# Performance work log

Measured on AMD Instinct MI355X. Metric: run time of the kernel, lower is better.

## Reference

```python
import jax, jax.numpy as jnp
import numpy as np

B, M, L, LQ, E, V = 32, 100, 30, 30, 256, 32000


def position_encoding(seq_len, emb):
    # faithful to MemN2N position encoding: 1 + 4*(k - (E+1)/2)*(j - (J+1)/2)/(E*J)
    j = jnp.arange(1, seq_len + 1, dtype=jnp.float32)[:, None]   # (J,1)
    k = jnp.arange(1, emb + 1, dtype=jnp.float32)[None, :]       # (1,E)
    half_e = (emb + 1) / 2.0
    half_j = (seq_len + 1) / 2.0
    return 1.0 + 4.0 * (k - half_e) * (j - half_j) / (emb * seq_len)  # (J,E)


def masked_softmax(x, m):
    xm = jnp.where(m > 0, x, -1e30)
    e = jnp.exp(xm - jnp.max(xm, axis=-1, keepdims=True)) * m
    return e / (jnp.sum(e, axis=-1, keepdims=True) + 1e-13)


def masked_log_softmax(x, m):
    return jax.nn.log_softmax(x + jnp.log(m + 1e-13), axis=-1)


def _forward(trainS, trainQ, trainVM, trainPM, trainSM, trainQM,
             A1, A2, A3, A4, W, b, gamma, beta):
    # query encoding: embed + position encode + query mask + sum over words
    Q = trainQ[:, 0, :]                                   # (B,LQ)
    pe_q = position_encoding(LQ, E)                       # (LQ,E)
    u = jnp.sum(A1[Q] * pe_q * trainQM[:, :, None], axis=1)  # (B,E)

    # story memory embeddings: gather + PE + sum over words.
    # NOTE: original code multiplies by trainSM but discards the result (bug),
    # so SM is intentionally NOT applied here.
    pe_s = position_encoding(L, E)                        # (L,E)
    embA1 = jnp.sum(A1[trainS] * pe_s, axis=2)            # (B,M,E)
    embA2 = jnp.sum(A2[trainS] * pe_s, axis=2)
    embA3 = jnp.sum(A3[trainS] * pe_s, axis=2)
    embA4 = jnp.sum(A4[trainS] * pe_s, axis=2)

    def hop(memA, memC, u):
        # scores = sum_E(memA * u) * PM (PM applied pre-sum is equivalent)
        scores = jnp.einsum('bme,be->bm', memA, u) * trainPM
        p = masked_softmax(scores, trainPM)               # (B,M)
        o = jnp.einsum('bm,bme->be', p, memC)             # (B,E)
        return o + u

    u = hop(embA1, embA2, u)   # hop 1
    u = hop(embA2, embA3, u)   # hop 2
    u = hop(embA3, embA4, u)   # hop 3

    # final linear + BatchNorm1d (training-mode batch stats, eps=1e-5)
    wx = u @ W.T + b                                      # (B,V)
    mean = jnp.mean(wx, axis=0)
    var = jnp.mean((wx - mean) ** 2, axis=0)
    y = gamma * (wx - mean) / jnp.sqrt(var + 1e-5) + beta
    return masked_log_softmax(y, trainVM)


def setup_inputs() -> dict:
    key = jax.random.key(0)
    ks = jax.random.split(key, 8)
    inp = {
        'trainS': jax.random.randint(ks[0], (B, M, L), 0, V, dtype=jnp.int32),
        'trainQ': jax.random.randint(ks[1], (B, 1, LQ), 0, V, dtype=jnp.int32),
        'trainVM': jnp.ones((B, V), jnp.float32),
        'trainPM': jnp.ones((B, M), jnp.float32),
        'trainSM': jnp.ones((B, M, L), jnp.float32),
        'trainQM': jnp.ones((B, LQ), jnp.float32),
        'A1': 0.1 * jax.random.normal(ks[2], (V, E), jnp.float32),
        'A2': 0.1 * jax.random.normal(ks[3], (V, E), jnp.float32),
        'A3': 0.1 * jax.random.normal(ks[4], (V, E), jnp.float32),
        'A4': 0.1 * jax.random.normal(ks[5], (V, E), jnp.float32),
        'W': jax.random.normal(ks[6], (V, E), jnp.float32) / np.sqrt(E),
        'b': jnp.zeros((V,), jnp.float32),
        'gamma': jnp.ones((V,), jnp.float32),
        'beta': jnp.zeros((V,), jnp.float32),
        'inspect': 0,
    }
    return inp


def reference(trainS, trainQ, trainVM, trainPM, trainSM, trainQM,
              A1, A2, A3, A4, W, b, gamma, beta, inspect):
    return _forward(trainS, trainQ, trainVM, trainPM, trainSM, trainQM,
                    A1, A2, A3, A4, W, b, gamma, beta)
```

## Files before the change

### kernel.cpp

```cpp
#include <hip/hip_runtime.h>
#include <math.h>

static constexpr int B_ = 32, M_ = 100, L_ = 30, LQ_ = 30, E_ = 256, V_ = 32000;

typedef __attribute__((ext_vector_type(8))) short bf16x8;
typedef __attribute__((ext_vector_type(4))) float f32x4;

__device__ __forceinline__ unsigned f2bf(float f) {
    unsigned u = __float_as_uint(f);
    return (u + 0x7FFFu + ((u >> 16) & 1u)) >> 16;
}

__global__ __launch_bounds__(256) void k_embed(const int* __restrict__ trainS,
                                               const float* __restrict__ A1,
                                               const float* __restrict__ A2,
                                               const float* __restrict__ A3,
                                               const float* __restrict__ A4,
                                               float* __restrict__ embA) {
    const int bm = blockIdx.x;
    const int tbl = threadIdx.x >> 6;
    const int e0 = (threadIdx.x & 63) * 4;
    const float* __restrict__ A = (tbl == 0) ? A1 : (tbl == 1) ? A2 : (tbl == 2) ? A3 : A4;
    const float half_e = (E_ + 1) * 0.5f;
    const float half_j = (L_ + 1) * 0.5f;
    const float inv = 1.0f / (float)(E_ * L_);
    const float k0 = (float)(e0 + 1) - half_e;
    const float k1 = k0 + 1.f, k2 = k0 + 2.f, k3 = k0 + 3.f;

    int idx[L_];
#pragma unroll
    for (int l = 0; l < L_; ++l) idx[l] = trainS[bm * L_ + l];

    float4 acc = make_float4(0.f, 0.f, 0.f, 0.f);
#pragma unroll
    for (int c = 0; c < 2; ++c) {
        float4 r[15];
#pragma unroll
        for (int j = 0; j < 15; ++j)
            r[j] = *reinterpret_cast<const float4*>(A + (size_t)idx[c * 15 + j] * E_ + e0);
        __builtin_amdgcn_sched_barrier(0);
#pragma unroll
        for (int j = 0; j < 15; ++j) {
            const int l = c * 15 + j;
            const float coef = 4.0f * ((float)(l + 1) - half_j) * inv;
            acc.x += r[j].x * (1.0f + coef * k0);
            acc.y += r[j].y * (1.0f + coef * k1);
            acc.z += r[j].z * (1.0f + coef * k2);
            acc.w += r[j].w * (1.0f + coef * k3);
        }
    }
    *reinterpret_cast<float4*>(embA + (size_t)tbl * (B_ * M_ * E_) + (size_t)bm * E_ + e0) = acc;
}

__global__ __launch_bounds__(1024) void k_hops(const int* __restrict__ trainQ,
                                               const float* __restrict__ trainQM,
                                               const float* __restrict__ A1,
                                               const float* __restrict__ embA,
                                               const float* __restrict__ trainPM,
                                               float* __restrict__ u_N,
                                               float* __restrict__ partial) {
    const int b = blockIdx.x;
    const int tid = threadIdx.x;
    const int lane = tid & 63;
    const int wave = tid >> 6;
    const int g = tid >> 8;
    const int e = tid & 255;
    if (tid < 8) partial[b * 8 + tid] = 0.f;
    __shared__ float u_sh[E_];
    __shared__ float sc[M_];
    __shared__ float p_sh[M_];
    __shared__ float osum[4][E_];

    {
        const float half_e = (E_ + 1) * 0.5f;
        const float half_j = (LQ_ + 1) * 0.5f;
        const float inv = 1.0f / (float)(E_ * LQ_);
        const float ke = (float)(e + 1) - half_e;
        const int l0 = g * 8;
        const int ln = (LQ_ - l0 < 8) ? (LQ_ - l0) : 8;
        int qi[8];
        float qm[8];
#pragma unroll
        for (int j = 0; j < 8; ++j) {
            if (j < ln) {
                qi[j] = trainQ[b * LQ_ + l0 + j];
                qm[j] = trainQM[b * LQ_ + l0 + j];
            } else { qi[j] = 0; qm[j] = 0.f; }
        }
        float r[8];
#pragma unroll
        for (int j = 0; j < 8; ++j)
            r[j] = (j < ln) ? A1[(size_t)qi[j] * E_ + e] : 0.f;
        float part = 0.f;
#pragma unroll
        for (int j = 0; j < 8; ++j) {
            const float pe = 1.0f + 4.0f * ke * ((float)(l0 + j + 1) - half_j) * inv;
            part += r[j] * pe * qm[j];
        }
        osum[g][e] = part;
    }
    __syncthreads();
    if (tid < E_) u_sh[tid] = osum[0][tid] + osum[1][tid] + osum[2][tid] + osum[3][tid];
    __syncthreads();

    for (int hop = 0; hop < 3; ++hop) {
        const float* memA = embA + (size_t)hop * (B_ * M_ * E_) + (size_t)b * M_ * E_;
        const float* memC = memA + (size_t)(B_ * M_ * E_);
#pragma unroll 2
        for (int m = wave; m < M_; m += 16) {
            const float* row = memA + m * E_;
            float part = 0.f;
#pragma unroll
            for (int j = 0; j < 4; ++j)
                part += row[lane + 64 * j] * u_sh[lane + 64 * j];
#pragma unroll
            for (int off = 32; off > 0; off >>= 1)
                part += __shfl_xor(part, off, 64);
            if (lane == 0) sc[m] = part * trainPM[b * M_ + m];
        }
        __syncthreads();
        if (wave == 0) {
            const float pm0 = (lane < M_) ? trainPM[b * M_ + lane] : 0.f;
            const float pm1 = (lane + 64 < M_) ? trainPM[b * M_ + lane + 64] : 0.f;
            const float x0 = (lane < M_ && pm0 > 0.f) ? sc[lane] : -1e30f;
            const float x1 = (lane + 64 < M_ && pm1 > 0.f) ? sc[lane + 64] : -1e30f;
            float mx = fmaxf(x0, x1);
#pragma unroll
            for (int off = 32; off > 0; off >>= 1)
                mx = fmaxf(mx, __shfl_xor(mx, off, 64));
            const float e0v = (lane < M_) ? expf(x0 - mx) * pm0 : 0.f;
            const float e1v = (lane + 64 < M_) ? expf(x1 - mx) * pm1 : 0.f;
            float ssum = e0v + e1v;
#pragma unroll
            for (int off = 32; off > 0; off >>= 1)
                ssum += __shfl_xor(ssum, off, 64);
            const float invs = 1.0f / (ssum + 1e-13f);
            if (lane < M_) p_sh[lane] = e0v * invs;
            if (lane + 64 < M_) p_sh[lane + 64] = e1v * invs;
        }
        __syncthreads();
        {
            float acc = 0.f;
            const float* crow = memC + e;
            const int m0 = g * 25;
#pragma unroll 5
            for (int mm = 0; mm < 25; ++mm)
                acc += p_sh[m0 + mm] * crow[(size_t)(m0 + mm) * E_];
            osum[g][e] = acc;
        }
        __syncthreads();
        if (tid < E_) u_sh[tid] += osum[0][tid] + osum[1][tid] + osum[2][tid] + osum[3][tid];
        __syncthreads();
    }
    if (tid < E_) u_N[b * E_ + tid] = u_sh[tid];
}

__global__ __launch_bounds__(256) void k_output(const float* __restrict__ u_N,
                                                const float* __restrict__ Wm,
                                                const float* __restrict__ gamma,
                                                const float* __restrict__ beta,
                                                const float* __restrict__ VM,
                                                float* __restrict__ z,
                                                float* __restrict__ partial) {
    __shared__ char uAraw[32 * 512];
    __shared__ float pex[B_];
    const int tid = threadIdx.x;
    {
        const int m = tid >> 3;
        const int kc = (tid & 7) * 32;
        const float4* src = reinterpret_cast<const float4*>(u_N + m * E_ + kc);
#pragma unroll
        for (int j = 0; j < 4; ++j) {
            const float4 f0 = src[2 * j];
            const float4 f1 = src[2 * j + 1];
            uint4 q;
            q.x = f2bf(f0.x) | (f2bf(f0.y) << 16);
            q.y = f2bf(f0.z) | (f2bf(f0.w) << 16);
            q.z = f2bf(f1.x) | (f2bf(f1.y) << 16);
            q.w = f2bf(f1.z) | (f2bf(f1.w) << 16);
            const int k16 = kc / 8 + j;
            const int off = m * 512 + ((k16 * 16) ^ ((m & 7) << 4));
            *reinterpret_cast<uint4*>(uAraw + off) = q;
        }
    }
    if (tid < B_) pex[tid] = 0.f;
    __syncthreads();

    const int lane = tid & 63;
    const int wv = tid >> 6;
    const int col = lane & 15;
    const int grp = lane >> 4;
    const int n0 = (blockIdx.x * 4 + wv) * 16;
    const int v = n0 + col;

    float4 wreg[16];
    {
        const float* wrow = Wm + (size_t)v * E_ + grp * 8;
#pragma unroll
        for (int s = 0; s < 8; ++s) {
            wreg[2 * s] = *reinterpret_cast<const float4*>(wrow + s * 32);
            wreg[2 * s + 1] = *reinterpret_cast<const float4*>(wrow + s * 32 + 4);
        }
    }
    __builtin_amdgcn_sched_barrier(0);

    bf16x8 af[2][8];
#pragma unroll
    for (int mt = 0; mt < 2; ++mt) {
        const int m = mt * 16 + col;
#pragma unroll
        for (int s = 0; s < 8; ++s) {
            const int k16 = s * 4 + grp;
            const int off = m * 512 + ((k16 * 16) ^ ((m & 7) << 4));
            af[mt][s] = *reinterpret_cast<bf16x8*>(uAraw + off);
        }
    }

    f32x4 acc0 = {0.f, 0.f, 0.f, 0.f};
    f32x4 acc1 = {0.f, 0.f, 0.f, 0.f};
#pragma unroll
    for (int s = 0; s < 8; ++s) {
        const float4 w0 = wreg[2 * s], w1 = wreg[2 * s + 1];
        bf16x8 bf;
        bf[0] = (short)f2bf(w0.x); bf[1] = (short)f2bf(w0.y);
        bf[2] = (short)f2bf(w0.z); bf[3] = (short)f2bf(w0.w);
        bf[4] = (short)f2bf(w1.x); bf[5] = (short)f2bf(w1.y);
        bf[6] = (short)f2bf(w1.z); bf[7] = (short)f2bf(w1.w);
        acc0 = __builtin_amdgcn_mfma_f32_16x16x32_bf16(af[0][s], bf, acc0, 0, 0, 0);
        acc1 = __builtin_amdgcn_mfma_f32_16x16x32_bf16(af[1][s], bf, acc1, 0, 0, 0);
    }

    float s1 = 0.f, s2 = 0.f;
#pragma unroll
    for (int r = 0; r < 4; ++r) {
        s1 += acc0[r] + acc1[r];
        s2 += acc0[r] * acc0[r] + acc1[r] * acc1[r];
    }
    s1 += __shfl_xor(s1, 16, 64);
    s2 += __shfl_xor(s2, 16, 64);
    s1 += __shfl_xor(s1, 32, 64);
    s2 += __shfl_xor(s2, 32, 64);
    const float mean = s1 * (1.0f / B_);
    const float var = s2 * (1.0f / B_) - mean * mean;
    const float rstd = rsqrtf(var + 1e-5f);
    const float gg = gamma[v], be = beta[v];

#pragma unroll
    for (int mt = 0; mt < 2; ++mt) {
#pragma unroll
        for (int r = 0; r < 4; ++r) {
            const int b = mt * 16 + grp * 4 + r;
            const float wx = (mt == 0) ? acc0[r] : acc1[r];
            const float y = gg * (wx - mean) * rstd + be;
            const size_t row = (size_t)b * V_ + v;
            const float vm = VM[row] + 1e-13f;
            z[row] = y + logf(vm);
            atomicAdd(&pex[b], vm * expf(y));
        }
    }
    __syncthreads();
    if (tid < B_) atomicAdd(&partial[tid * 8 + (blockIdx.x & 7)], pex[tid]);
}

__global__ __launch_bounds__(256) void k_final(const float* __restrict__ z,
                                               const float* __restrict__ partial,
                                               float* __restrict__ out) {
    const int idx = blockIdx.x * 256 + threadIdx.x;
    const int b = idx / (V_ / 4);
    const int v4 = idx % (V_ / 4);
    float s = 0.f;
#pragma unroll
    for (int k = 0; k < 8; ++k) s += partial[b * 8 + k];
    const float lse = logf(s);
    const float4 x = reinterpret_cast<const float4*>(z + (size_t)b * V_)[v4];
    float4 o;
    o.x = x.x - lse; o.y = x.y - lse; o.z = x.z - lse; o.w = x.w - lse;
    reinterpret_cast<float4*>(out + (size_t)b * V_)[v4] = o;
}

extern "C" void kernel_launch(void* const* d_in, const int* in_sizes, int n_in,
                              void* d_out, int out_size, void* d_ws, size_t ws_size,
                              hipStream_t stream) {
    const int* trainS = (const int*)d_in[0];
    const int* trainQ = (const int*)d_in[1];
    const float* trainVM = (const float*)d_in[2];
    const float* trainPM = (const float*)d_in[3];
    const float* trainQM = (const float*)d_in[5];
    const float* A1 = (const float*)d_in[6];
    const float* A2 = (const float*)d_in[7];
    const float* A3 = (const float*)d_in[8];
    const float* A4 = (const float*)d_in[9];
    const float* Wm = (const float*)d_in[10];
    const float* gamma = (const float*)d_in[12];
    const float* beta = (const float*)d_in[13];
    float* out = (float*)d_out;

    float* ws = (float*)d_ws;
    float* u_N = ws;
    float* embA = ws + 8192;
    float* z = embA + 4 * (B_ * M_ * E_);
    float* partial = z + (size_t)B_ * V_;

    k_embed<<<B_ * M_, 256, 0, stream>>>(trainS, A1, A2, A3, A4, embA);
    k_hops<<<B_, 1024, 0, stream>>>(trainQ, trainQM, A1, embA, trainPM, u_N, partial);
    k_output<<<V_ / 64, 256, 0, stream>>>(u_N, Wm, gamma, beta, trainVM, z, partial);
    k_final<<<(B_ * V_ / 4) / 256, 256, 0, stream>>>(z, partial, out);
}
```

Before: 108.9 us.

## Split output GEMM batch halves across waves and reduce exp sums via shuffles

In k_output, each block now covers 32 vocab columns instead of 64, and each wave computes one 16-row batch half of one 16-column tile. This doubles the grid and halves the per-wave MFMA and epilogue work. BatchNorm statistics are combined across wave pairs through shared memory with an extra barrier. The per-element shared-memory atomics for the softmax denominator are replaced by shuffle reductions followed by one atomic per row group. The trade-off is that each W row is now loaded by two waves, adding redundant global traffic, plus the added block-level sync.

New measurement: 118.2 us. 1.09x slower.

```diff
diff --git a/kernel.cpp b/kernel.cpp
--- a/kernel.cpp
+++ b/kernel.cpp
@@ -164,6 +164,7 @@
                                                 float* __restrict__ partial) {
     __shared__ char uAraw[32 * 512];
     __shared__ float pex[B_];
+    __shared__ float pairStat[2][2][16][2];
     const int tid = threadIdx.x;
     {
         const int m = tid >> 3;
@@ -188,10 +189,11 @@
 
     const int lane = tid & 63;
     const int wv = tid >> 6;
+    const int p = wv >> 1;
+    const int mt = wv & 1;
     const int col = lane & 15;
     const int grp = lane >> 4;
-    const int n0 = (blockIdx.x * 4 + wv) * 16;
-    const int v = n0 + col;
+    const int v = blockIdx.x * 32 + p * 16 + col;
 
     float4 wreg[16];
     {
@@ -204,20 +206,18 @@
     }
     __builtin_amdgcn_sched_barrier(0);
 
-    bf16x8 af[2][8];
-#pragma unroll
-    for (int mt = 0; mt < 2; ++mt) {
+    bf16x8 af[8];
+    {
         const int m = mt * 16 + col;
 #pragma unroll
         for (int s = 0; s < 8; ++s) {
             const int k16 = s * 4 + grp;
             const int off = m * 512 + ((k16 * 16) ^ ((m & 7) << 4));
-            af[mt][s] = *reinterpret_cast<bf16x8*>(uAraw + off);
-        }
-    }
-
-    f32x4 acc0 = {0.f, 0.f, 0.f, 0.f};
-    f32x4 acc1 = {0.f, 0.f, 0.f, 0.f};
+            af[s] = *reinterpret_cast<bf16x8*>(uAraw + off);
+        }
+    }
+
+    f32x4 acc = {0.f, 0.f, 0.f, 0.f};
 #pragma unroll
     for (int s = 0; s < 8; ++s) {
         const float4 w0 = wreg[2 * s], w1 = wreg[2 * s + 1];
@@ -226,37 +226,46 @@
         bf[2] = (short)f2bf(w0.z); bf[3] = (short)f2bf(w0.w);
         bf[4] = (short)f2bf(w1.x); bf[5] = (short)f2bf(w1.y);
         bf[6] = (short)f2bf(w1.z); bf[7] = (short)f2bf(w1.w);
-        acc0 = __builtin_amdgcn_mfma_f32_16x16x32_bf16(af[0][s], bf, acc0, 0, 0, 0);
-        acc1 = __builtin_amdgcn_mfma_f32_16x16x32_bf16(af[1][s], bf, acc1, 0, 0, 0);
-    }
-
-    float s1 = 0.f, s2 = 0.f;
-#pragma unroll
-    for (int r = 0; r < 4; ++r) {
-        s1 += acc0[r] + acc1[r];
-        s2 += acc0[r] * acc0[r] + acc1[r] * acc1[r];
-    }
+        acc = __builtin_amdgcn_mfma_f32_16x16x32_bf16(af[s], bf, acc, 0, 0, 0);
+    }
+
+    float s1 = acc[0] + acc[1] + acc[2] + acc[3];
+    float s2 = acc[0] * acc[0] + acc[1] * acc[1] + acc[2] * acc[2] + acc[3] * acc[3];
     s1 += __shfl_xor(s1, 16, 64);
     s2 += __shfl_xor(s2, 16, 64);
     s1 += __shfl_xor(s1, 32, 64);
     s2 += __shfl_xor(s2, 32, 64);
-    const float mean = s1 * (1.0f / B_);
-    const float var = s2 * (1.0f / B_) - mean * mean;
+    if (lane < 16) {
+        pairStat[p][mt][col][0] = s1;
+        pairStat[p][mt][col][1] = s2;
+    }
+    __syncthreads();
+    const float S1 = pairStat[p][0][col][0] + pairStat[p][1][col][0];
+    const float S2 = pairStat[p][0][col][1] + pairStat[p][1][col][1];
+    const float mean = S1 * (1.0f / B_);
+    const float var = S2 * (1.0f / B_) - mean * mean;
     const float rstd = rsqrtf(var + 1e-5f);
     const float gg = gamma[v], be = beta[v];
 
-#pragma unroll
-    for (int mt = 0; mt < 2; ++mt) {
-#pragma unroll
-        for (int r = 0; r < 4; ++r) {
-            const int b = mt * 16 + grp * 4 + r;
-            const float wx = (mt == 0) ? acc0[r] : acc1[r];
-            const float y = gg * (wx - mean) * rstd + be;
-            const size_t row = (size_t)b * V_ + v;
-            const float vm = VM[row] + 1e-13f;
-            z[row] = y + logf(vm);
-            atomicAdd(&pex[b], vm * expf(y));
-        }
+    float ex[4];
+#pragma unroll
+    for (int r = 0; r < 4; ++r) {
+        const int b = mt * 16 + grp * 4 + r;
+        const float y = gg * (acc[r] - mean) * rstd + be;
+        const size_t row = (size_t)b * V_ + v;
+        const float vm = VM[row] + 1e-13f;
+        z[row] = y + logf(vm);
+        ex[r] = vm * expf(y);
+    }
+#pragma unroll
+    for (int off = 1; off < 16; off <<= 1) {
+#pragma unroll
+        for (int r = 0; r < 4; ++r) ex[r] += __shfl_xor(ex[r], off, 64);
+    }
+    if (col == 0) {
+#pragma unroll
+        for (int r = 0; r < 4; ++r)
+            atomicAdd(&pex[mt * 16 + grp * 4 + r], ex[r]);
     }
     __syncthreads();
     if (tid < B_) atomicAdd(&partial[tid * 8 + (blockIdx.x & 7)], pex[tid]);
@@ -303,6 +312,6 @@
 
     k_embed<<<B_ * M_, 256, 0, stream>>>(trainS, A1, A2, A3, A4, embA);
     k_hops<<<B_, 1024, 0, stream>>>(trainQ, trainQM, A1, embA, trainPM, u_N, partial);
-    k_output<<<V_ / 64, 256, 0, stream>>>(u_N, Wm, gamma, beta, trainVM, z, partial);
+    k_output<<<V_ / 32, 256, 0, stream>>>(u_N, Wm, gamma, beta, trainVM, z, partial);
     k_final<<<(B_ * V_ / 4) / 256, 256, 0, stream>>>(z, partial, out);
 }
```

## Split embedding gather into per-table launches with word-split waves and LDS reduction

Applied to the files above, without the earlier changes.

The single embedding kernel, where each wave handled one table across all 30 words, is replaced by four launches, one per table. Within each block the four waves split the 30 words into chunks of 8 and reduce the partial sums through shared memory. Each table's working set stays more cache-local within a launch, and per-thread register pressure drops from 15 in-flight float4 loads to 8. The cost is three extra kernel launches, a block barrier, and some padded dummy loads in the last wave.

After: 111.7 us. 1.03x slower.

```diff
diff --git a/kernel.cpp b/kernel.cpp
--- a/kernel.cpp
+++ b/kernel.cpp
@@ -11,45 +11,46 @@
     return (u + 0x7FFFu + ((u >> 16) & 1u)) >> 16;
 }
 
-__global__ __launch_bounds__(256) void k_embed(const int* __restrict__ trainS,
-                                               const float* __restrict__ A1,
-                                               const float* __restrict__ A2,
-                                               const float* __restrict__ A3,
-                                               const float* __restrict__ A4,
-                                               float* __restrict__ embA) {
+__global__ __launch_bounds__(256) void k_embed_t(const int* __restrict__ trainS,
+                                                 const float* __restrict__ A,
+                                                 float* __restrict__ embT) {
     const int bm = blockIdx.x;
-    const int tbl = threadIdx.x >> 6;
+    const int w = threadIdx.x >> 6;
     const int e0 = (threadIdx.x & 63) * 4;
-    const float* __restrict__ A = (tbl == 0) ? A1 : (tbl == 1) ? A2 : (tbl == 2) ? A3 : A4;
+    __shared__ float osum[4][E_];
     const float half_e = (E_ + 1) * 0.5f;
     const float half_j = (L_ + 1) * 0.5f;
     const float inv = 1.0f / (float)(E_ * L_);
     const float k0 = (float)(e0 + 1) - half_e;
     const float k1 = k0 + 1.f, k2 = k0 + 2.f, k3 = k0 + 3.f;
-
-    int idx[L_];
-#pragma unroll
-    for (int l = 0; l < L_; ++l) idx[l] = trainS[bm * L_ + l];
+    const int l0 = w * 8;
+    const int ln = (L_ - l0 < 8) ? (L_ - l0) : 8;
+
+    int idx[8];
+#pragma unroll
+    for (int j = 0; j < 8; ++j)
+        idx[j] = trainS[bm * L_ + l0 + ((j < ln) ? j : 0)];
+    float4 r[8];
+#pragma unroll
+    for (int j = 0; j < 8; ++j)
+        r[j] = *reinterpret_cast<const float4*>(A + (size_t)idx[j] * E_ + e0);
+    __builtin_amdgcn_sched_barrier(0);
 
     float4 acc = make_float4(0.f, 0.f, 0.f, 0.f);
 #pragma unroll
-    for (int c = 0; c < 2; ++c) {
-        float4 r[15];
-#pragma unroll
-        for (int j = 0; j < 15; ++j)
-            r[j] = *reinterpret_cast<const float4*>(A + (size_t)idx[c * 15 + j] * E_ + e0);
-        __builtin_amdgcn_sched_barrier(0);
-#pragma unroll
-        for (int j = 0; j < 15; ++j) {
-            const int l = c * 15 + j;
-            const float coef = 4.0f * ((float)(l + 1) - half_j) * inv;
-            acc.x += r[j].x * (1.0f + coef * k0);
-            acc.y += r[j].y * (1.0f + coef * k1);
-            acc.z += r[j].z * (1.0f + coef * k2);
-            acc.w += r[j].w * (1.0f + coef * k3);
-        }
-    }
-    *reinterpret_cast<float4*>(embA + (size_t)tbl * (B_ * M_ * E_) + (size_t)bm * E_ + e0) = acc;
+    for (int j = 0; j < 8; ++j) {
+        const int l = l0 + j;
+        const float on = (j < ln) ? 1.0f : 0.0f;
+        const float coef = on * 4.0f * ((float)(l + 1) - half_j) * inv;
+        acc.x += r[j].x * (on + coef * k0);
+        acc.y += r[j].y * (on + coef * k1);
+        acc.z += r[j].z * (on + coef * k2);
+        acc.w += r[j].w * (on + coef * k3);
+    }
+    *reinterpret_cast<float4*>(&osum[w][e0]) = acc;
+    __syncthreads();
+    const int e = threadIdx.x;
+    embT[(size_t)bm * E_ + e] = osum[0][e] + osum[1][e] + osum[2][e] + osum[3][e];
 }
 
 __global__ __launch_bounds__(1024) void k_hops(const int* __restrict__ trainQ,
@@ -301,7 +302,9 @@
     float* z = embA + 4 * (B_ * M_ * E_);
     float* partial = z + (size_t)B_ * V_;
 
-    k_embed<<<B_ * M_, 256, 0, stream>>>(trainS, A1, A2, A3, A4, embA);
+    const float* tabs[4] = {A1, A2, A3, A4};
+    for (int t = 0; t < 4; ++t)
+        k_embed_t<<<B_ * M_, 256, 0, stream>>>(trainS, tabs[t], embA + (size_t)t * (B_ * M_ * E_));
     k_hops<<<B_, 1024, 0, stream>>>(trainQ, trainQM, A1, embA, trainPM, u_N, partial);
     k_output<<<V_ / 64, 256, 0, stream>>>(u_N, Wm, gamma, beta, trainVM, z, partial);
     k_final<<<(B_ * V_ / 4) / 256, 256, 0, stream>>>(z, partial, out);
```

## Pre-sort story word indices per sentence to improve gather locality in embed

Applied to the files above, without the earlier changes.

Adds a kernel that bitonic-sorts each sentence's 30 word indices, packing the token id and the original position into one int, so that the embedding gather in k_embed visits table rows in ascending address order. k_embed unpacks the position to recompute the position-encoding coefficient and now processes the gathers in chunks of 8 instead of 15. The aim is better cache and DRAM locality on the random gathers, at the cost of an extra kernel launch and an extra index buffer round trip. The packing assumes index*32 fits in an int, which holds for V=32000.

New measurement: 116.3 us. 6.8% more time.

```diff
diff --git a/kernel.cpp b/kernel.cpp
--- a/kernel.cpp
+++ b/kernel.cpp
@@ -11,7 +11,28 @@
     return (u + 0x7FFFu + ((u >> 16) & 1u)) >> 16;
 }
 
-__global__ __launch_bounds__(256) void k_embed(const int* __restrict__ trainS,
+__global__ __launch_bounds__(256) void k_sortidx(const int* __restrict__ trainS,
+                                                 int* __restrict__ sortedS) {
+    const int lane = threadIdx.x & 63;
+    const int bm = blockIdx.x * 4 + (threadIdx.x >> 6);
+    int v = 0x7FFFFFFF;
+    if (lane < L_) v = trainS[bm * L_ + lane] * 32 + lane;
+#pragma unroll
+    for (int k = 2; k <= 64; k <<= 1) {
+#pragma unroll
+        for (int j = k >> 1; j >= 1; j >>= 1) {
+            const int p = __shfl_xor(v, j, 64);
+            const bool up = (lane & k) == 0;
+            const bool lower = (lane & j) == 0;
+            const int mn = (v < p) ? v : p;
+            const int mx = (v < p) ? p : v;
+            v = (lower == up) ? mn : mx;
+        }
+    }
+    if (lane < L_) sortedS[bm * L_ + lane] = v;
+}
+
+__global__ __launch_bounds__(256) void k_embed(const int* __restrict__ sortedS,
                                                const float* __restrict__ A1,
                                                const float* __restrict__ A2,
                                                const float* __restrict__ A3,
@@ -27,28 +48,39 @@
     const float k0 = (float)(e0 + 1) - half_e;
     const float k1 = k0 + 1.f, k2 = k0 + 2.f, k3 = k0 + 3.f;
 
-    int idx[L_];
-#pragma unroll
-    for (int l = 0; l < L_; ++l) idx[l] = trainS[bm * L_ + l];
+    int pk[L_];
+#pragma unroll
+    for (int l = 0; l < L_; ++l) pk[l] = sortedS[bm * L_ + l];
 
     float4 acc = make_float4(0.f, 0.f, 0.f, 0.f);
-#pragma unroll
-    for (int c = 0; c < 2; ++c) {
-        float4 r[15];
-#pragma unroll
-        for (int j = 0; j < 15; ++j)
-            r[j] = *reinterpret_cast<const float4*>(A + (size_t)idx[c * 15 + j] * E_ + e0);
-        __builtin_amdgcn_sched_barrier(0);
-#pragma unroll
-        for (int j = 0; j < 15; ++j) {
-            const int l = c * 15 + j;
-            const float coef = 4.0f * ((float)(l + 1) - half_j) * inv;
-            acc.x += r[j].x * (1.0f + coef * k0);
-            acc.y += r[j].y * (1.0f + coef * k1);
-            acc.z += r[j].z * (1.0f + coef * k2);
-            acc.w += r[j].w * (1.0f + coef * k3);
-        }
-    }
+
+#define PROC_CHUNK(J0, N)                                                         \
+    {                                                                             \
+        float4 r[8];                                                              \
+        float cl[8];                                                              \
+        _Pragma("unroll")                                                         \
+        for (int j = 0; j < (N); ++j) {                                           \
+            const int p = pk[(J0) + j];                                           \
+            r[j] = *reinterpret_cast<const float4*>(A + (size_t)(p >> 5) * E_ + e0); \
+            cl[j] = (float)((p & 31) + 1) - half_j;                               \
+        }                                                                         \
+        __builtin_amdgcn_sched_barrier(0);                                        \
+        _Pragma("unroll")                                                         \
+        for (int j = 0; j < (N); ++j) {                                           \
+            const float coef = 4.0f * cl[j] * inv;                                \
+            acc.x += r[j].x * (1.0f + coef * k0);                                 \
+            acc.y += r[j].y * (1.0f + coef * k1);                                 \
+            acc.z += r[j].z * (1.0f + coef * k2);                                 \
+            acc.w += r[j].w * (1.0f + coef * k3);                                 \
+        }                                                                         \
+    }
+
+    PROC_CHUNK(0, 8)
+    PROC_CHUNK(8, 8)
+    PROC_CHUNK(16, 8)
+    PROC_CHUNK(24, 6)
+#undef PROC_CHUNK
+
     *reinterpret_cast<float4*>(embA + (size_t)tbl * (B_ * M_ * E_) + (size_t)bm * E_ + e0) = acc;
 }
 
@@ -300,8 +332,10 @@
     float* embA = ws + 8192;
     float* z = embA + 4 * (B_ * M_ * E_);
     float* partial = z + (size_t)B_ * V_;
-
-    k_embed<<<B_ * M_, 256, 0, stream>>>(trainS, A1, A2, A3, A4, embA);
+    int* sortedS = (int*)(partial + 256);
+
+    k_sortidx<<<B_ * M_ / 4, 256, 0, stream>>>(trainS, sortedS);
+    k_embed<<<B_ * M_, 256, 0, stream>>>(sortedS, A1, A2, A3, A4, embA);
     k_hops<<<B_, 1024, 0, stream>>>(trainQ, trainQM, A1, embA, trainPM, u_N, partial);
     k_output<<<V_ / 64, 256, 0, stream>>>(u_N, Wm, gamma, beta, trainVM, z, partial);
     k_final<<<(B_ * V_ / 4) / 256, 256, 0, stream>>>(z, partial, out);
```
